# Optimization experiments

Hardware: AMD Instinct MI355X
Metric: run time of the kernel (lower is better)

## Reference

```python
import jax, jax.numpy as jnp
import numpy as np
from jax import lax

B = 32  # CS block size


def _conv(x, w, stride=1, pad=0):
    return lax.conv_general_dilated(
        x, w, window_strides=(stride, stride),
        padding=[(pad, pad), (pad, pad)],
        dimension_numbers=("NCHW", "OIHW", "NCHW"))


def _prelu(x, a):
    return jnp.where(x >= 0, x, a * x)


def _reshape_concat(x):
    # x: [N, B*B, h, w]; channel c = j*B + i maps to block pixel (i, j)
    # (tmp.view(B,B).permute(1,0) in the torch code). Blocks tile rows by
    # dim2 (h) and cols by dim3 (w). Vectorized depth-to-space + transpose.
    N, C, h, w = x.shape
    x5 = x.reshape(N, B, B, h, w)            # dims: (N, j, i, h, w)
    x5 = jnp.transpose(x5, (0, 3, 2, 4, 1))  # (N, h, i, w, j)
    return x5.reshape(N, 1, h * B, w * B)


def setup_inputs() -> dict:
    key = jax.random.key(0)
    ks = jax.random.split(key, 6)
    N, H, W = 16, 256, 256
    csnb = int(0.25 * B * B)  # 256
    inp = {
        "x": jax.random.normal(ks[0], (N, 1, H, W), jnp.float32),
        "W_cs": jax.random.normal(ks[1], (csnb, 1, B, B), jnp.float32) * 0.03,
        "W_init": jax.random.normal(ks[2], (B * B, csnb, 1, 1), jnp.float32) * 0.06,
        "W_first": jax.random.normal(ks[3], (64, 1, 3, 3), jnp.float32) * 0.3,
        "W_blk": jax.random.normal(ks[4], (64, 64, 3, 3), jnp.float32) * 0.04,
        "W_last": jax.random.normal(ks[5], (1, 64, 3, 3), jnp.float32) * 0.04,
        "a_main": jnp.full((1,), 0.1, jnp.float32),
        "a_blk": jnp.full((1,), 0.1, jnp.float32),
    }
    return inp


def reference(x, W_cs, W_init, W_first, W_blk, W_last, a_main, a_blk):
    # CS sampling: [N,1,H,W] -> [N,csnb,H/B,W/B]
    outcsy = _conv(x, W_cs, stride=B, pad=0)
    # initial reconstruction: 1x1 conv to B*B channels
    out = _conv(outcsy, W_init, stride=1, pad=0)
    out_initrec = _reshape_concat(out)          # [N,1,H,W]
    out = _prelu(_conv(out_initrec, W_first, pad=1), a_main)
    # same SORTRes_block (shared weights) applied 4 times
    for _ in range(4):
        o1 = _conv(out, W_blk, pad=1)
        o2 = _prelu(o1, a_blk)
        o3 = _conv(o2, W_blk, pad=1)
        out = _prelu(out + o3, a_blk)
    out = _conv(out + out_initrec, W_last, pad=1)
    return (out, outcsy, out_initrec)
```

## Files before the change

kernel.cpp:

```cpp
#include <hip/hip_runtime.h>
#include <hip/hip_bf16.h>
#include <initializer_list>


#define HW 65536
#define IMG 4194304

typedef __attribute__((ext_vector_type(8))) short short8;
typedef __attribute__((ext_vector_type(4))) short short4v;
typedef __attribute__((ext_vector_type(4))) float f32x4;

__device__ __forceinline__ float bf2f(unsigned short u) {
    union { unsigned u; float f; } v; v.u = ((unsigned)u) << 16; return v.f;
}
__device__ __forceinline__ unsigned short f2bf(float f) {
    union { float f; unsigned u; } v; v.f = f;
    unsigned r = v.u + 0x7FFF + ((v.u >> 16) & 1);
    return (unsigned short)(r >> 16);
}

__global__ void k_wcsT(const float* __restrict__ Wcs, float* __restrict__ WT)
{
    int e = blockIdx.x * 256 + threadIdx.x;
    int k = e >> 8, c = e & 255;
    WT[(long)k * 256 + c] = Wcs[(long)c * 1024 + k];
}

__global__ void k_winitT(const float* __restrict__ Wi, float* __restrict__ WT)
{
    int e = blockIdx.x * 256 + threadIdx.x;
    int ci = e >> 10, cc = e & 1023;
    WT[e] = Wi[(long)cc * 256 + ci];
}

__global__ __launch_bounds__(256) void k_cs2(const float* __restrict__ x,
        const float* __restrict__ WT, float* __restrict__ outcsy)
{
    __shared__ float xs[2][1024];
    const int b = blockIdx.x;
    const int tid = threadIdx.x;
#pragma unroll
    for (int t = 0; t < 2; ++t) {
        int p = b * 2 + t;
        int wb = p & 7, hb = (p >> 3) & 7, n = p >> 6;
#pragma unroll
        for (int i = 0; i < 4; ++i) {
            int k = tid + 256 * i;
            int ii = k >> 5, jj = k & 31;
            xs[t][k] = x[(long)n * HW + (hb * 32 + ii) * 256 + wb * 32 + jj];
        }
    }
    __syncthreads();
    float a0 = 0.f, a1 = 0.f;
    for (int k = 0; k < 1024; k += 8) {
#pragma unroll
        for (int u = 0; u < 8; ++u) {
            float wv = WT[(long)(k + u) * 256 + tid];
            a0 += wv * xs[0][k + u];
            a1 += wv * xs[1][k + u];
        }
    }
#pragma unroll
    for (int t = 0; t < 2; ++t) {
        int p = b * 2 + t;
        int wb = p & 7, hb = (p >> 3) & 7, n = p >> 6;
        float a = t ? a1 : a0;
        outcsy[(long)n * 16384 + tid * 64 + hb * 8 + wb] = a;
    }
}

__global__ __launch_bounds__(256) void k_init2(const float* __restrict__ outcsy,
        const float* __restrict__ WT, float* __restrict__ initrec)
{
    __shared__ float ys[2][256];
    __shared__ float ov[2][1024];
    const int b = blockIdx.x;
    const int np = b & 7, s = b >> 3;
    const int wb = s & 7, hb = s >> 3;
    const int tid = threadIdx.x;
#pragma unroll
    for (int i = 0; i < 2; ++i) {
        int idx = tid + 256 * i;
        int t = idx >> 8, c = idx & 255;
        ys[t][c] = outcsy[(long)(np * 2 + t) * 16384 + c * 64 + s];
    }
    __syncthreads();
#pragma unroll
    for (int q4 = 0; q4 < 4; ++q4) {
        int cc = q4 * 256 + tid;
        float a0 = 0.f, a1 = 0.f;
        for (int ci = 0; ci < 256; ci += 8) {
#pragma unroll
            for (int u = 0; u < 8; ++u) {
                float wv = WT[(long)(ci + u) * 1024 + cc];
                a0 += wv * ys[0][ci + u];
                a1 += wv * ys[1][ci + u];
            }
        }
        int i = cc & 31, j = cc >> 5;
        ov[0][i * 32 + j] = a0;
        ov[1][i * 32 + j] = a1;
    }
    __syncthreads();
#pragma unroll
    for (int t = 0; t < 2; ++t) {
        int n = np * 2 + t;
#pragma unroll
        for (int i2 = 0; i2 < 4; ++i2) {
            int p = i2 * 256 + tid;
            int i = p >> 5, j = p & 31;
            initrec[(long)n * HW + (hb * 32 + i) * 256 + wb * 32 + j] = ov[t][p];
        }
    }
}

__global__ __launch_bounds__(256) void k_first(const float* __restrict__ initrec,
        const float* __restrict__ Wf, unsigned short* __restrict__ A,
        const float* __restrict__ alpha_p)
{
    const int bid = blockIdx.x;
    const int tx = bid & 15, ty = (bid >> 4) & 15, n = bid >> 8;
    const int tid = threadIdx.x;
    const int x = (tx << 4) + (tid & 15), y = (ty << 4) + (tid >> 4);
    const float* ip = initrec + (long)n * HW;

    float in[9];
#pragma unroll
    for (int ky = 0; ky < 3; ++ky)
#pragma unroll
        for (int kx = 0; kx < 3; ++kx) {
            int iy = y + ky - 1, ix = x + kx - 1;
            in[ky * 3 + kx] = ((unsigned)iy < 256u && (unsigned)ix < 256u)
                                  ? ip[iy * 256 + ix] : 0.f;
        }

    const float alpha = alpha_p[0];
    unsigned short* op = &A[(((long)n * 256 + y) * 256 + x) * 64];
#pragma unroll
    for (int c8 = 0; c8 < 8; ++c8) {
        short8 ov;
#pragma unroll
        for (int j = 0; j < 8; ++j) {
            const float* wp = &Wf[(c8 * 8 + j) * 9];
            float a = 0.f;
#pragma unroll
            for (int t = 0; t < 9; ++t) a += wp[t] * in[t];
            a = a >= 0.f ? a : alpha * a;
            ov[j] = (short)f2bf(a);
        }
        *(short8*)&op[c8 * 8] = ov;
    }
}

__global__ void k_wprep(const float* __restrict__ Wb, unsigned short* __restrict__ Wp)
{
    int e = blockIdx.x * 256 + threadIdx.x;
    int buf = e / 36864, r0 = e % 36864;
    int cc = r0 / 18432, r = r0 % 18432;
    int tap = r / 2048, r2 = r % 2048;
    int nt = (r2 >> 9) & 3, l = (r2 >> 3) & 63, j = r2 & 7;
    int co = nt * 16 + (l & 15);
    int k = cc * 32 + (l >> 4) * 8 + j;
    int ci = buf ? ((k & 3) * 16 + (k >> 2)) : k;
    Wp[e] = f2bf(Wb[co * 576 + ci * 9 + tap]);
}

__global__ __launch_bounds__(256, 3) void k_res(const unsigned short* __restrict__ src,
        unsigned short* __restrict__ dst, const unsigned short* __restrict__ WpAll,
        const float* __restrict__ alpha_p)
{
    __shared__ short smem[23328];

    const int tid = threadIdx.x;
    const int bid = blockIdx.x;
    const int tx = bid & 15, ty = (bid >> 4) & 15, n = bid >> 8;
    const int x0 = tx * 16, y0 = ty * 16;
    const int w = tid >> 6, lane = tid & 63;
    const int q = lane >> 4, mm = lane & 15;
    const float alpha = alpha_p[0];
    const unsigned short* sb = src + (long)n * IMG;

    int pb1[6];
#pragma unroll
    for (int i = 0; i < 6; ++i) {
        int p = (w + 4 * i) * 16 + mm;
        p = p < 323 ? p : 323;
        pb1[i] = p + 2 * (p / 18);
    }

    short8 bcur[4], bnxt[4];
#pragma unroll
    for (int nt = 0; nt < 4; ++nt)
        bcur[nt] = *(const short8*)&WpAll[(size_t)((nt * 512) + lane * 8)];

    const f32x4 zz = {0.f, 0.f, 0.f, 0.f};
    f32x4 acc1[6][4];
#pragma unroll
    for (int i = 0; i < 6; ++i)
#pragma unroll
        for (int nt = 0; nt < 4; ++nt) acc1[i][nt] = zz;

    for (int cc = 0; cc < 2; ++cc) {
        if (cc) __syncthreads();
#pragma unroll
        for (int i = 0; i < 7; ++i) {
            int idx = tid + 256 * i;
            if (idx < 1600) {
                int pix = idx >> 2, part = idx & 3;
                int row = pix / 20, col = pix - row * 20;
                int gy = y0 + row - 2, gx = x0 + col - 2;
                short8 v = {0, 0, 0, 0, 0, 0, 0, 0};
                if ((unsigned)gy < 256u && (unsigned)gx < 256u)
                    v = *(const short8*)&sb[((long)gy * 256 + gx) * 64 + cc * 32 + part * 8];
                *(short8*)&smem[pix * 40 + part * 8] = v;
            }
        }
        __syncthreads();

#pragma unroll
        for (int tap = 0; tap < 9; ++tap) {
            const int un = cc * 9 + tap + 1;
            const int ub = un / 18, um = un % 18;
#pragma unroll
            for (int nt = 0; nt < 4; ++nt)
                bnxt[nt] = *(const short8*)&WpAll[(size_t)ub * 36864 +
                           (size_t)(um / 9) * 18432 +
                           (size_t)(((um % 9) * 4 + nt) * 512 + lane * 8)];
            const int ky = tap / 3, kx = tap % 3;
            const int toff = (ky * 20 + kx) * 40 + q * 8;
#pragma unroll
            for (int i = 0; i < 6; ++i) {
                short8 af = *(const short8*)&smem[pb1[i] * 40 + toff];
#pragma unroll
                for (int nt = 0; nt < 4; ++nt)
                    acc1[i][nt] = __builtin_amdgcn_mfma_f32_16x16x32_bf16(
                        af, bcur[nt], acc1[i][nt], 0, 0, 0);
            }
#pragma unroll
            for (int nt = 0; nt < 4; ++nt) bcur[nt] = bnxt[nt];
        }
    }
    __syncthreads();

#pragma unroll
    for (int i = 0; i < 6; ++i) {
        int t = w + 4 * i;
        if (t < 21) {
#pragma unroll
            for (int r = 0; r < 4; ++r) {
                int p = t * 16 + q * 4 + r;
                p = p < 323 ? p : 323;
                int rho = p / 18, gam = p - 18 * rho;
                bool valid = (unsigned)(y0 - 1 + rho) < 256u &&
                             (unsigned)(x0 - 1 + gam) < 256u;
                short4v ov;
#pragma unroll
                for (int nt = 0; nt < 4; ++nt) {
                    float v = acc1[i][nt][r];
                    v = v >= 0.f ? v : alpha * v;
                    ov[nt] = valid ? (short)f2bf(v) : (short)0;
                }
                *(short4v*)&smem[p * 72 + mm * 4] = ov;
            }
        }
    }
    __syncthreads();

    f32x4 acc2[4][4];
#pragma unroll
    for (int mt = 0; mt < 4; ++mt)
#pragma unroll
        for (int nt = 0; nt < 4; ++nt) acc2[mt][nt] = zz;

    for (int cc = 0; cc < 2; ++cc) {
#pragma unroll
        for (int tap = 0; tap < 9; ++tap) {
            const int un0 = 18 + cc * 9 + tap + 1;
            const int un = un0 < 36 ? un0 : 35;
            const int um = un % 18;
#pragma unroll
            for (int nt = 0; nt < 4; ++nt)
                bnxt[nt] = *(const short8*)&WpAll[(size_t)36864 +
                           (size_t)(um / 9) * 18432 +
                           (size_t)(((um % 9) * 4 + nt) * 512 + lane * 8)];
            const int ky = tap / 3, kx = tap % 3;
#pragma unroll
            for (int mt = 0; mt < 4; ++mt) {
                short8 af = *(const short8*)&smem[((4 * w + mt + ky) * 18 + mm + kx) * 72 +
                                                  cc * 32 + q * 8];
#pragma unroll
                for (int nt = 0; nt < 4; ++nt)
                    acc2[mt][nt] = __builtin_amdgcn_mfma_f32_16x16x32_bf16(
                        af, bcur[nt], acc2[mt][nt], 0, 0, 0);
            }
#pragma unroll
            for (int nt = 0; nt < 4; ++nt) bcur[nt] = bnxt[nt];
        }
    }
    __syncthreads();

    unsigned short* ob = (unsigned short*)smem;
#pragma unroll
    for (int mt = 0; mt < 4; ++mt) {
        int row = 4 * w + mt;
#pragma unroll
        for (int nt = 0; nt < 4; ++nt)
#pragma unroll
            for (int r = 0; r < 4; ++r) {
                int xx = q * 4 + r;
                ob[(row * 16 + xx) * 64 + nt * 16 + mm] = f2bf(acc2[mt][nt][r]);
            }
    }
    __syncthreads();
#pragma unroll
    for (int i = 0; i < 8; ++i) {
        int e = (tid + 256 * i) * 8;
        int co = e & 63, xx = (e >> 6) & 15, row = e >> 10;
        long g = (((long)n * 256 + y0 + row) * 256 + (x0 + xx)) * 64 + co;
        short8 cv = *(short8*)&ob[e];
        short8 rv = *(const short8*)&src[(long)n * IMG +
                                         ((long)(y0 + row) * 256 + x0 + xx) * 64 + co];
        short8 ov;
#pragma unroll
        for (int j = 0; j < 8; ++j) {
            float v = bf2f((unsigned short)cv[j]) + bf2f((unsigned short)rv[j]);
            v = (v >= 0.f) ? v : alpha * v;
            ov[j] = (short)f2bf(v);
        }
        *(short8*)&dst[(long)n * IMG + ((long)(y0 + row) * 256 + x0 + xx) * 64 + co] = ov;
    }
}

__global__ __launch_bounds__(256) void k_last(const unsigned short* __restrict__ A,
        const float* __restrict__ initrec, const float* __restrict__ Wl,
        float* __restrict__ out0)
{
    __shared__ short ibuf[23328];
    const int bid = blockIdx.x;
    const int tx = bid & 15, ty = (bid >> 4) & 15, n = bid >> 8;
    const int x0 = tx * 16, y0 = ty * 16;
    const int tid = threadIdx.x;
    const unsigned short* Ab = A + (long)n * IMG;

#pragma unroll
    for (int i = 0; i < 11; ++i) {
        int idx = tid + 256 * i;
        if (idx < 2592) {
            int pix = idx >> 3, part = idx & 7;
            int row = pix / 18, col = pix - row * 18;
            int gy = y0 + row - 1, gx = x0 + col - 1;
            short8 v = {0, 0, 0, 0, 0, 0, 0, 0};
            if ((unsigned)gy < 256u && (unsigned)gx < 256u)
                v = *(const short8*)&Ab[((long)gy * 256 + gx) * 64 + part * 8];
            *(short8*)&ibuf[pix * 72 + part * 8] = v;
        }
    }
    __syncthreads();

    float wsum[9];
#pragma unroll
    for (int k = 0; k < 9; ++k) wsum[k] = 0.f;
    for (int ci = 0; ci < 64; ++ci)
#pragma unroll
        for (int k = 0; k < 9; ++k) wsum[k] += Wl[ci * 9 + k];

    const int x = tid & 15, y = tid >> 4;
    const float* ip = initrec + (long)n * HW;
    float acc = 0.f;
#pragma unroll
    for (int ky = 0; ky < 3; ++ky) {
#pragma unroll
        for (int kx = 0; kx < 3; ++kx) {
            const int tap = ky * 3 + kx;
            const short* p = &ibuf[((y + ky) * 18 + (x + kx)) * 72];
#pragma unroll
            for (int c8 = 0; c8 < 8; ++c8) {
                short8 av = *(const short8*)&p[c8 * 8];
#pragma unroll
                for (int j = 0; j < 8; ++j)
                    acc += Wl[(c8 * 8 + j) * 9 + tap] * bf2f((unsigned short)av[j]);
            }
            int gy = y0 + y + ky - 1, gx = x0 + x + kx - 1;
            if ((unsigned)gy < 256u && (unsigned)gx < 256u)
                acc += wsum[tap] * ip[gy * 256 + gx];
        }
    }
    out0[((long)n * 256 + y0 + y) * 256 + (x0 + x)] = acc;
}

extern "C" void kernel_launch(void* const* d_in, const int* in_sizes, int n_in,
                              void* d_out, int out_size, void* d_ws, size_t ws_size,
                              hipStream_t stream)
{
    const float* x     = (const float*)d_in[0];
    const float* Wcs   = (const float*)d_in[1];
    const float* Winit = (const float*)d_in[2];
    const float* Wf    = (const float*)d_in[3];
    const float* Wb    = (const float*)d_in[4];
    const float* Wl    = (const float*)d_in[5];
    const float* amain = (const float*)d_in[6];
    const float* ablk  = (const float*)d_in[7];

    float* out0    = (float*)d_out;
    float* outcsy  = out0 + 1048576;
    float* initrec = outcsy + 262144;

    const size_t EXTRA = 147456 + 2 * 1048576;
    unsigned short* A = (unsigned short*)d_ws;
    int nc = 1;
    for (int c : {16, 8, 4, 2, 1})
        if ((size_t)(16 + c) * IMG * 2 + EXTRA <= ws_size) { nc = c; break; }
    unsigned short* Bt   = A + (size_t)16 * IMG;
    unsigned short* Wp   = Bt + (size_t)nc * IMG;
    float*          WcsT = (float*)(Wp + 73728);
    float*          WinT = WcsT + 262144;

    k_wcsT<<<1024, 256, 0, stream>>>(Wcs, WcsT);
    k_winitT<<<1024, 256, 0, stream>>>(Winit, WinT);
    k_wprep<<<288, 256, 0, stream>>>(Wb, Wp);

    k_cs2<<<512, 256, 0, stream>>>(x, WcsT, outcsy);
    k_init2<<<512, 256, 0, stream>>>(outcsy, WinT, initrec);
    k_first<<<4096, 256, 0, stream>>>(initrec, Wf, A, amain);

    for (int n0 = 0; n0 < 16; n0 += nc) {
        unsigned short* Ac = A + (size_t)n0 * IMG;
        for (int i = 0; i < 4; ++i) {
            const unsigned short* s = (i & 1) ? Bt : Ac;
            unsigned short*       d = (i & 1) ? Ac : Bt;
            k_res<<<nc * 256, 256, 0, stream>>>(s, d, Wp, ablk);
        }
    }
    k_last<<<4096, 256, 0, stream>>>(A, initrec, Wl, out0);
}
```

Baseline: 1.302 ms.

## Store activations in permuted channel order to vectorize residual epilogue stores

Activations are now stored in a permuted channel order, the same interleaving that conv2 already used. k_first and k_last remap their weights to match, and one set of packed weights serves both convs in k_res. This lets the conv2 epilogue write four channels per pixel with one short4 store instead of scattered 2-byte LDS stores, and halves the weight prep buffer. The batch chunk limit also drops from 16 to 8 images, which adds an extra outer iteration when the workspace would have allowed 16.

After: 1.339 ms. 1.03x slower.

```diff
diff --git a/kernel.cpp b/kernel.cpp
--- a/kernel.cpp
+++ b/kernel.cpp
@@ -137,36 +137,37 @@
     const float alpha = alpha_p[0];
     unsigned short* op = &A[(((long)n * 256 + y) * 256 + x) * 64];
 #pragma unroll
-    for (int c8 = 0; c8 < 8; ++c8) {
+    for (int s8 = 0; s8 < 8; ++s8) {
         short8 ov;
 #pragma unroll
         for (int j = 0; j < 8; ++j) {
-            const float* wp = &Wf[(c8 * 8 + j) * 9];
+            int slot = s8 * 8 + j;
+            int c = (slot & 3) * 16 + (slot >> 2);
+            const float* wp = &Wf[c * 9];
             float a = 0.f;
 #pragma unroll
             for (int t = 0; t < 9; ++t) a += wp[t] * in[t];
             a = a >= 0.f ? a : alpha * a;
             ov[j] = (short)f2bf(a);
         }
-        *(short8*)&op[c8 * 8] = ov;
+        *(short8*)&op[s8 * 8] = ov;
     }
 }
 
 __global__ void k_wprep(const float* __restrict__ Wb, unsigned short* __restrict__ Wp)
 {
     int e = blockIdx.x * 256 + threadIdx.x;
-    int buf = e / 36864, r0 = e % 36864;
-    int cc = r0 / 18432, r = r0 % 18432;
+    int cc = e / 18432, r = e % 18432;
     int tap = r / 2048, r2 = r % 2048;
     int nt = (r2 >> 9) & 3, l = (r2 >> 3) & 63, j = r2 & 7;
     int co = nt * 16 + (l & 15);
     int k = cc * 32 + (l >> 4) * 8 + j;
-    int ci = buf ? ((k & 3) * 16 + (k >> 2)) : k;
+    int ci = (k & 3) * 16 + (k >> 2);
     Wp[e] = f2bf(Wb[co * 576 + ci * 9 + tap]);
 }
 
 __global__ __launch_bounds__(256, 3) void k_res(const unsigned short* __restrict__ src,
-        unsigned short* __restrict__ dst, const unsigned short* __restrict__ WpAll,
+        unsigned short* __restrict__ dst, const unsigned short* __restrict__ Wp,
         const float* __restrict__ alpha_p)
 {
     __shared__ short smem[23328];
@@ -191,7 +192,7 @@
     short8 bcur[4], bnxt[4];
 #pragma unroll
     for (int nt = 0; nt < 4; ++nt)
-        bcur[nt] = *(const short8*)&WpAll[(size_t)((nt * 512) + lane * 8)];
+        bcur[nt] = *(const short8*)&Wp[(size_t)(nt * 512 + lane * 8)];
 
     const f32x4 zz = {0.f, 0.f, 0.f, 0.f};
     f32x4 acc1[6][4];
@@ -219,13 +220,12 @@
 
 #pragma unroll
         for (int tap = 0; tap < 9; ++tap) {
-            const int un = cc * 9 + tap + 1;
-            const int ub = un / 18, um = un % 18;
+            int un = cc * 9 + tap + 1;
+            un = un < 18 ? un : 0;
 #pragma unroll
             for (int nt = 0; nt < 4; ++nt)
-                bnxt[nt] = *(const short8*)&WpAll[(size_t)ub * 36864 +
-                           (size_t)(um / 9) * 18432 +
-                           (size_t)(((um % 9) * 4 + nt) * 512 + lane * 8)];
+                bnxt[nt] = *(const short8*)&Wp[(size_t)(un / 9) * 18432 +
+                           (size_t)(((un % 9) * 4 + nt) * 512 + lane * 8)];
             const int ky = tap / 3, kx = tap % 3;
             const int toff = (ky * 20 + kx) * 40 + q * 8;
 #pragma unroll
@@ -275,14 +275,12 @@
     for (int cc = 0; cc < 2; ++cc) {
 #pragma unroll
         for (int tap = 0; tap < 9; ++tap) {
-            const int un0 = 18 + cc * 9 + tap + 1;
-            const int un = un0 < 36 ? un0 : 35;
-            const int um = un % 18;
+            int un = cc * 9 + tap + 1;
+            un = un < 18 ? un : 17;
 #pragma unroll
             for (int nt = 0; nt < 4; ++nt)
-                bnxt[nt] = *(const short8*)&WpAll[(size_t)36864 +
-                           (size_t)(um / 9) * 18432 +
-                           (size_t)(((um % 9) * 4 + nt) * 512 + lane * 8)];
+                bnxt[nt] = *(const short8*)&Wp[(size_t)(un / 9) * 18432 +
+                           (size_t)(((un % 9) * 4 + nt) * 512 + lane * 8)];
             const int ky = tap / 3, kx = tap % 3;
 #pragma unroll
             for (int mt = 0; mt < 4; ++mt) {
@@ -304,22 +302,24 @@
     for (int mt = 0; mt < 4; ++mt) {
         int row = 4 * w + mt;
 #pragma unroll
-        for (int nt = 0; nt < 4; ++nt)
-#pragma unroll
-            for (int r = 0; r < 4; ++r) {
-                int xx = q * 4 + r;
-                ob[(row * 16 + xx) * 64 + nt * 16 + mm] = f2bf(acc2[mt][nt][r]);
-            }
+        for (int r = 0; r < 4; ++r) {
+            int px = row * 16 + q * 4 + r;
+            short4v ov;
+#pragma unroll
+            for (int nt = 0; nt < 4; ++nt)
+                ov[nt] = (short)f2bf(acc2[mt][nt][r]);
+            *(short4v*)&ob[px * 64 + mm * 4] = ov;
+        }
     }
     __syncthreads();
 #pragma unroll
     for (int i = 0; i < 8; ++i) {
         int e = (tid + 256 * i) * 8;
-        int co = e & 63, xx = (e >> 6) & 15, row = e >> 10;
-        long g = (((long)n * 256 + y0 + row) * 256 + (x0 + xx)) * 64 + co;
+        int sl = e & 63, xx = (e >> 6) & 15, row = e >> 10;
+        long g = (((long)n * 256 + y0 + row) * 256 + (x0 + xx)) * 64 + sl;
         short8 cv = *(short8*)&ob[e];
         short8 rv = *(const short8*)&src[(long)n * IMG +
-                                         ((long)(y0 + row) * 256 + x0 + xx) * 64 + co];
+                                         ((long)(y0 + row) * 256 + x0 + xx) * 64 + sl];
         short8 ov;
 #pragma unroll
         for (int j = 0; j < 8; ++j) {
@@ -327,7 +327,7 @@
             v = (v >= 0.f) ? v : alpha * v;
             ov[j] = (short)f2bf(v);
         }
-        *(short8*)&dst[(long)n * IMG + ((long)(y0 + row) * 256 + x0 + xx) * 64 + co] = ov;
+        *(short8*)&dst[(long)n * IMG + ((long)(y0 + row) * 256 + x0 + xx) * 64 + sl] = ov;
     }
 }
 
@@ -377,8 +377,11 @@
             for (int c8 = 0; c8 < 8; ++c8) {
                 short8 av = *(const short8*)&p[c8 * 8];
 #pragma unroll
-                for (int j = 0; j < 8; ++j)
-                    acc += Wl[(c8 * 8 + j) * 9 + tap] * bf2f((unsigned short)av[j]);
+                for (int j = 0; j < 8; ++j) {
+                    int slot = c8 * 8 + j;
+                    int ci = (slot & 3) * 16 + (slot >> 2);
+                    acc += Wl[ci * 9 + tap] * bf2f((unsigned short)av[j]);
+                }
             }
             int gy = y0 + y + ky - 1, gx = x0 + x + kx - 1;
             if ((unsigned)gy < 256u && (unsigned)gx < 256u)
@@ -405,19 +408,19 @@
     float* outcsy  = out0 + 1048576;
     float* initrec = outcsy + 262144;
 
-    const size_t EXTRA = 147456 + 2 * 1048576;
+    const size_t EXTRA = 73728 + 2 * 1048576;
     unsigned short* A = (unsigned short*)d_ws;
     int nc = 1;
-    for (int c : {16, 8, 4, 2, 1})
+    for (int c : {8, 4, 2, 1})
         if ((size_t)(16 + c) * IMG * 2 + EXTRA <= ws_size) { nc = c; break; }
     unsigned short* Bt   = A + (size_t)16 * IMG;
     unsigned short* Wp   = Bt + (size_t)nc * IMG;
-    float*          WcsT = (float*)(Wp + 73728);
+    float*          WcsT = (float*)(Wp + 36864);
     float*          WinT = WcsT + 262144;
 
     k_wcsT<<<1024, 256, 0, stream>>>(Wcs, WcsT);
     k_winitT<<<1024, 256, 0, stream>>>(Winit, WinT);
-    k_wprep<<<288, 256, 0, stream>>>(Wb, Wp);
+    k_wprep<<<144, 256, 0, stream>>>(Wb, Wp);
 
     k_cs2<<<512, 256, 0, stream>>>(x, WcsT, outcsy);
     k_init2<<<512, 256, 0, stream>>>(outcsy, WinT, initrec);
```
